# Optimization experiments

Measured on AMD Instinct MI355X. Metric: run time of the kernel, lower is better.

## Reference

```python
import jax, jax.numpy as jnp
import numpy as np

BETA = 0.9
THR = 1.0
NUM_STEPS = 10
SLOPE = 25.0


def spike(x):
    # forward-only heaviside (surrogate grad handled in fwdbwd module)
    return (x > 0).astype(x.dtype)


def setup_inputs() -> dict:
    key = jax.random.key(0)
    ks = jax.random.split(key, 7)
    B = 131072
    x = jax.random.normal(ks[0], (B, 250), dtype=jnp.float32)
    W1 = jax.random.normal(ks[1], (256, 250), dtype=jnp.float32) * 0.06
    b1 = jax.random.normal(ks[2], (256,), dtype=jnp.float32) * 0.06
    W2 = jax.random.normal(ks[3], (128, 256), dtype=jnp.float32) * 0.06
    b2 = jax.random.normal(ks[4], (128,), dtype=jnp.float32) * 0.06
    W3 = jax.random.normal(ks[5], (5, 128), dtype=jnp.float32) * 0.09
    b3 = jax.random.normal(ks[6], (5,), dtype=jnp.float32) * 0.09
    return {"x": x, "W1": W1, "b1": b1, "W2": W2, "b2": b2, "W3": W3, "b3": b3}


def reference(x, W1, b1, W2, b2, W3, b3):
    B = x.shape[0]
    # cur1 is identical every step (input x is static) -> hoist out of loop
    cur1 = x @ W1.T + b1  # [B, 256]

    def step(carry, _):
        m1, m2, m3, acc = carry
        # snntorch Leaky (reset_mechanism='subtract'):
        # reset from incoming mem (detached), then decay+input-reset, then fire
        r1 = (m1 > THR).astype(x.dtype)
        m1 = BETA * m1 + cur1 - r1 * THR
        s1 = spike(m1 - THR)

        cur2 = s1 @ W2.T + b2  # [B, 128]
        r2 = (m2 > THR).astype(x.dtype)
        m2 = BETA * m2 + cur2 - r2 * THR
        s2 = spike(m2 - THR)

        cur3 = s2 @ W3.T + b3  # [B, 5]
        r3 = (m3 > THR).astype(x.dtype)
        m3 = BETA * m3 + cur3 - r3 * THR
        s3 = spike(m3 - THR)

        return (m1, m2, m3, acc + s3), None

    init = (
        jnp.zeros((B, 256), x.dtype),
        jnp.zeros((B, 128), x.dtype),
        jnp.zeros((B, 5), x.dtype),
        jnp.zeros((B, 5), x.dtype),
    )
    (_, _, _, acc), _ = jax.lax.scan(step, init, None, length=NUM_STEPS)
    return acc  # sum of output spikes over timesteps, [B, 5]
```

## Files before the change

### kernel.cpp

```cpp
#include <hip/hip_runtime.h>

#define NSTEP 10

typedef __attribute__((ext_vector_type(8))) short bf16x8;
typedef __attribute__((ext_vector_type(4))) float f32x4;

extern "C" __global__ void __launch_bounds__(256) snn_prep(
    const float* __restrict__ W1, float* __restrict__ W1T)
{
    int i0 = blockIdx.x * 256 + threadIdx.x;
    int stride = gridDim.x * 256;
    for (int idx = i0; idx < 250 * 256; idx += stride) {
        int k = idx >> 8;
        int n = idx & 255;
        W1T[idx] = W1[n * 250 + k];
    }
}

__device__ __forceinline__ unsigned int bf16_rne_hi(float f) {
    unsigned int u = __float_as_uint(f);
    return (u + 0x7FFFu + ((u >> 16) & 1u)) & 0xFFFF0000u;
}

extern "C" __global__ void __launch_bounds__(256) snn_prep2(
    const float* __restrict__ W2, unsigned short* __restrict__ W2F)
{
    int idx = blockIdx.x * 256 + threadIdx.x;
    if (idx >= 8 * 3 * 8 * 64) return;
    int lane  = idx & 63;
    int slab  = (idx >> 6) & 7;
    int split = (idx >> 9) % 3;
    int w     = idx / (3 * 8 * 64);
    int j  = w * 16 + (lane & 15);
    int k0 = slab * 32 + (lane >> 4) * 8;
    unsigned short res[8];
    #pragma unroll
    for (int e = 0; e < 8; ++e) {
        float wval = W2[j * 256 + k0 + e];
        unsigned int u1 = bf16_rne_hi(wval);
        float r1 = __fsub_rn(wval, __uint_as_float(u1));
        unsigned int u2 = bf16_rne_hi(r1);
        float r2 = __fsub_rn(r1, __uint_as_float(u2));
        unsigned int u3 = bf16_rne_hi(r2);
        unsigned int sel = (split == 0) ? u1 : (split == 1) ? u2 : u3;
        res[e] = (unsigned short)(sel >> 16);
    }
    *(uint4*)&W2F[(((w * 3 + split) * 8 + slab) << 9) + lane * 8] =
        *(uint4*)res;
}

extern "C" __global__ void __launch_bounds__(256) snn_cur1(
    const float* __restrict__ x,
    const float* __restrict__ b1,
    const float* __restrict__ W1T,
    float* __restrict__ curG)
{
    __shared__ __align__(16) float xT[250 * 36];
    __shared__ __align__(16) float W1c[25 * 256];
    const int t   = threadIdx.x;
    const int nt  = t & 15;
    const int st  = t >> 4;
    const int s0a = st * 2;
    const int nt4 = nt * 4;
    const int sBase = blockIdx.x * 32;

    for (int i = t; i < 32 * 250; i += 256) {
        int sl = i / 250;
        int kl = i - sl * 250;
        xT[kl * 36 + sl] = x[(sBase + sl) * 250 + kl];
    }

    float rs[25];
    #pragma unroll
    for (int j = 0; j < 25; ++j) rs[j] = W1T[j * 256 + t];

    float cur1[4][4][2];
    #pragma unroll
    for (int j = 0; j < 4; ++j)
        #pragma unroll
        for (int e = 0; e < 4; ++e) { cur1[j][e][0] = 0.0f; cur1[j][e][1] = 0.0f; }

    __syncthreads();

    for (int c = 0; c < 10; ++c) {
        #pragma unroll
        for (int j = 0; j < 25; ++j) W1c[j * 256 + t] = rs[j];
        if (c < 9) {
            const float* src = W1T + (c + 1) * 6400;
            #pragma unroll
            for (int j = 0; j < 25; ++j) rs[j] = src[j * 256 + t];
        }
        __syncthreads();

        #pragma unroll 5
        for (int kl = 0; kl < 25; ++kl) {
            const int k = c * 25 + kl;
            const float2 xp = *(const float2*)&xT[k * 36 + s0a];
            float w[16];
            *(float4*)&w[0]  = *(const float4*)&W1c[kl * 256 +   0 + nt4];
            *(float4*)&w[4]  = *(const float4*)&W1c[kl * 256 +  64 + nt4];
            *(float4*)&w[8]  = *(const float4*)&W1c[kl * 256 + 128 + nt4];
            *(float4*)&w[12] = *(const float4*)&W1c[kl * 256 + 192 + nt4];
            #pragma unroll
            for (int j = 0; j < 4; ++j)
                #pragma unroll
                for (int e = 0; e < 4; ++e) {
                    cur1[j][e][0] = fmaf(w[j * 4 + e], xp.x, cur1[j][e][0]);
                    cur1[j][e][1] = fmaf(w[j * 4 + e], xp.y, cur1[j][e][1]);
                }
        }
        if (c < 9) __syncthreads();
    }

    {
        float bb[16];
        #pragma unroll
        for (int j = 0; j < 4; ++j)
            *(float4*)&bb[j * 4] = *(const float4*)&b1[j * 64 + nt4];
        #pragma unroll
        for (int j = 0; j < 4; ++j)
            #pragma unroll
            for (int e = 0; e < 4; ++e) {
                cur1[j][e][0] = __fadd_rn(cur1[j][e][0], bb[j * 4 + e]);
                cur1[j][e][1] = __fadd_rn(cur1[j][e][1], bb[j * 4 + e]);
            }
    }
    #pragma unroll
    for (int s = 0; s < 2; ++s)
        #pragma unroll
        for (int j = 0; j < 4; ++j) {
            *(float4*)&curG[(size_t)(sBase + s0a + s) * 256 + j * 64 + nt4] =
                make_float4(cur1[j][0][s], cur1[j][1][s],
                            cur1[j][2][s], cur1[j][3][s]);
        }
}

extern "C" __global__ void __launch_bounds__(512, 2) snn_main_split(
    const float* __restrict__ curG,
    const float* __restrict__ b2g,
    const float* __restrict__ W3,
    const float* __restrict__ b3,
    const unsigned short* __restrict__ W2F,
    float* __restrict__ out)
{
    __shared__ __align__(16) char ldsraw[51736];
    char* s1bf = ldsraw;
    unsigned char* s2Lb = (unsigned char*)(ldsraw + 32768);
    float* W3L = (float*)(ldsraw + 41984);
    float* pL  = (float*)(ldsraw + 46080);
    float* bL  = (float*)(ldsraw + 51200);

    const int t    = threadIdx.x;
    const int nt   = t & 15;
    const int st   = t >> 4;
    const int s0a  = st * 2;
    const int n0   = nt * 16;
    const int lane = t & 63;
    const int wv   = t >> 6;
    const int l15  = lane & 15;
    const int lq   = lane >> 4;
    const int sBase = blockIdx.x * 64;

    float cur1[16][2];
    #pragma unroll
    for (int s = 0; s < 2; ++s) {
        const float4* cp =
            (const float4*)&curG[(size_t)(sBase + s0a + s) * 256 + n0];
        float4 a = cp[0], b = cp[1], c = cp[2], d = cp[3];
        cur1[0][s] = a.x;  cur1[1][s] = a.y;  cur1[2][s] = a.z;  cur1[3][s] = a.w;
        cur1[4][s] = b.x;  cur1[5][s] = b.y;  cur1[6][s] = b.z;  cur1[7][s] = b.w;
        cur1[8][s] = c.x;  cur1[9][s] = c.y;  cur1[10][s] = c.z; cur1[11][s] = c.w;
        cur1[12][s] = d.x; cur1[13][s] = d.y; cur1[14][s] = d.z; cur1[15][s] = d.w;
    }

    for (int idx = t; idx < 640; idx += 512) {
        int o = idx >> 7;
        int j = idx & 127;
        W3L[j * 8 + o] = W3[idx];
    }
    if (t < 128) bL[t] = b2g[t];
    if (t < 5)   bL[128 + t] = b3[t];
    __syncthreads();

    float m1[16][2];
    #pragma unroll
    for (int i = 0; i < 16; ++i) { m1[i][0] = 0.0f; m1[i][1] = 0.0f; }
    float m2[4][4];
    #pragma unroll
    for (int mt = 0; mt < 4; ++mt)
        #pragma unroll
        for (int rg = 0; rg < 4; ++rg) m2[mt][rg] = 0.0f;
    float m3 = 0.0f, acc3 = 0.0f;

    const unsigned short* fb = W2F + (wv * 24) * 512 + lane * 8;
    const int keyB   = (lane & 7) << 4;
    const int chunkq = lq << 4;
    const int jC     = wv * 16 + l15;
    const int keyC2  = ((jC >> 2) & 7) << 3;

    #pragma unroll 1
    for (int stp = 0; stp < NSTEP; ++stp) {
        {
            unsigned int dwa[2][8];
            #pragma unroll
            for (int i = 0; i < 16; ++i) {
                #pragma unroll
                for (int s = 0; s < 2; ++s) {
                    float m = m1[i][s];
                    float r = (m > 1.0f) ? 1.0f : 0.0f;
                    m = __fsub_rn(__fadd_rn(__fmul_rn(0.9f, m), cur1[i][s]), r);
                    m1[i][s] = m;
                    unsigned int bits = (m > 1.0f) ? 0x3F80u : 0u;
                    if (i & 1) dwa[s][i >> 1] |= bits << 16;
                    else       dwa[s][i >> 1]  = bits;
                }
            }
            #pragma unroll
            for (int s = 0; s < 2; ++s) {
                const int row = s0a + s;
                const int key = row & 7;
                char* rp = s1bf + row * 512;
                uint4 lo = make_uint4(dwa[s][0], dwa[s][1], dwa[s][2], dwa[s][3]);
                uint4 hi = make_uint4(dwa[s][4], dwa[s][5], dwa[s][6], dwa[s][7]);
                *(uint4*)(rp + (((2 * nt + 0) ^ key) << 4)) = lo;
                *(uint4*)(rp + (((2 * nt + 1) ^ key) << 4)) = hi;
            }
        }
        __syncthreads();

        f32x4 acc[4];
        {
            const f32x4 z = {0.0f, 0.0f, 0.0f, 0.0f};
            acc[0] = z; acc[1] = z; acc[2] = z; acc[3] = z;
        }
        #pragma unroll
        for (int slab = 0; slab < 8; ++slab) {
            const bf16x8 B2 = *(const bf16x8*)(fb + (16 + slab) * 512);
            const bf16x8 B1 = *(const bf16x8*)(fb + (8  + slab) * 512);
            const bf16x8 B0 = *(const bf16x8*)(fb + (0  + slab) * 512);
            const int coff = (slab * 64 + chunkq) ^ keyB;
            const bf16x8 A0 = *(const bf16x8*)(s1bf + (l15     ) * 512 + coff);
            const bf16x8 A1 = *(const bf16x8*)(s1bf + (l15 + 16) * 512 + coff);
            const bf16x8 A2 = *(const bf16x8*)(s1bf + (l15 + 32) * 512 + coff);
            const bf16x8 A3 = *(const bf16x8*)(s1bf + (l15 + 48) * 512 + coff);
            acc[0] = __builtin_amdgcn_mfma_f32_16x16x32_bf16(A0, B2, acc[0], 0, 0, 0);
            acc[1] = __builtin_amdgcn_mfma_f32_16x16x32_bf16(A1, B2, acc[1], 0, 0, 0);
            acc[2] = __builtin_amdgcn_mfma_f32_16x16x32_bf16(A2, B2, acc[2], 0, 0, 0);
            acc[3] = __builtin_amdgcn_mfma_f32_16x16x32_bf16(A3, B2, acc[3], 0, 0, 0);
            acc[0] = __builtin_amdgcn_mfma_f32_16x16x32_bf16(A0, B1, acc[0], 0, 0, 0);
            acc[1] = __builtin_amdgcn_mfma_f32_16x16x32_bf16(A1, B1, acc[1], 0, 0, 0);
            acc[2] = __builtin_amdgcn_mfma_f32_16x16x32_bf16(A2, B1, acc[2], 0, 0, 0);
            acc[3] = __builtin_amdgcn_mfma_f32_16x16x32_bf16(A3, B1, acc[3], 0, 0, 0);
            acc[0] = __builtin_amdgcn_mfma_f32_16x16x32_bf16(A0, B0, acc[0], 0, 0, 0);
            acc[1] = __builtin_amdgcn_mfma_f32_16x16x32_bf16(A1, B0, acc[1], 0, 0, 0);
            acc[2] = __builtin_amdgcn_mfma_f32_16x16x32_bf16(A2, B0, acc[2], 0, 0, 0);
            acc[3] = __builtin_amdgcn_mfma_f32_16x16x32_bf16(A3, B0, acc[3], 0, 0, 0);
        }

        {
            const float bj = bL[jC];
            #pragma unroll
            for (int mt = 0; mt < 4; ++mt) {
                unsigned int pk = 0;
                #pragma unroll
                for (int rg = 0; rg < 4; ++rg) {
                    float c2 = __fadd_rn(acc[mt][rg], bj);
                    float m = m2[mt][rg];
                    float r = (m > 1.0f) ? 1.0f : 0.0f;
                    m = __fsub_rn(__fadd_rn(__fmul_rn(0.9f, m), c2), r);
                    m2[mt][rg] = m;
                    if (m > 1.0f) pk |= 1u << (8 * rg);
                }
                const int smp0 = mt * 16 + lq * 4;
                *(unsigned int*)&s2Lb[jC * 72 + (smp0 ^ keyC2)] = pk;
            }
        }
        __syncthreads();

        if (t < 256) {
            const int sl = t & 63;
            const int jr = t >> 6;
            float part[5] = {0.0f, 0.0f, 0.0f, 0.0f, 0.0f};
            #pragma unroll 8
            for (int jj = 0; jj < 32; ++jj) {
                const int j = jr * 32 + jj;
                const float s2v =
                    (float)s2Lb[j * 72 + (sl ^ (((j >> 2) & 7) << 3))];
                const float4 w3a = *(const float4*)&W3L[j * 8];
                const float  w3e = W3L[j * 8 + 4];
                part[0] = fmaf(w3a.x, s2v, part[0]);
                part[1] = fmaf(w3a.y, s2v, part[1]);
                part[2] = fmaf(w3a.z, s2v, part[2]);
                part[3] = fmaf(w3a.w, s2v, part[3]);
                part[4] = fmaf(w3e,   s2v, part[4]);
            }
            #pragma unroll
            for (int o = 0; o < 5; ++o)
                pL[(o * 4 + jr) * 64 + sl] = part[o];
        }
        __syncthreads();

        if (t < 320) {
            const int o  = t >> 6;
            const int sl = t & 63;
            float c3 = pL[(o * 4 + 0) * 64 + sl];
            c3 += pL[(o * 4 + 1) * 64 + sl];
            c3 += pL[(o * 4 + 2) * 64 + sl];
            c3 += pL[(o * 4 + 3) * 64 + sl];
            c3 = __fadd_rn(c3, bL[128 + o]);
            float m = m3;
            float r = (m > 1.0f) ? 1.0f : 0.0f;
            m = __fsub_rn(__fadd_rn(__fmul_rn(0.9f, m), c3), r);
            m3 = m;
            if (m > 1.0f) acc3 += 1.0f;
        }
    }

    if (t < 320) {
        out[(sBase + (t & 63)) * 5 + (t >> 6)] = acc3;
    }
}

extern "C" __global__ void __launch_bounds__(512, 2) snn_main_fused(
    const float* __restrict__ x,
    const float* __restrict__ b1,
    const float* __restrict__ b2g,
    const float* __restrict__ W3,
    const float* __restrict__ b3,
    const float* __restrict__ W1T,
    const unsigned short* __restrict__ W2F,
    float* __restrict__ out)
{
    __shared__ __align__(16) char ldsraw[68000];
    char* s1bf = ldsraw;
    unsigned char* s2Lb = (unsigned char*)(ldsraw + 32768);
    float* W3L = (float*)(ldsraw + 41984);
    float* pL  = (float*)(ldsraw + 46080);
    float* bL  = (float*)(ldsraw + 51200);
    float* xT  = (float*)(ldsraw);

    const int t    = threadIdx.x;
    const int nt   = t & 15;
    const int st   = t >> 4;
    const int s0a  = st * 2;
    const int n0   = nt * 16;
    const int lane = t & 63;
    const int wv   = t >> 6;
    const int l15  = lane & 15;
    const int lq   = lane >> 4;
    const int sBase = blockIdx.x * 64;

    for (int i = t; i < 64 * 250; i += 512) {
        int sl = i / 250;
        int kl = i - sl * 250;
        xT[kl * 68 + sl] = x[(sBase + sl) * 250 + kl];
    }
    __syncthreads();

    float cur1[16][2];
    #pragma unroll
    for (int i = 0; i < 16; ++i) { cur1[i][0] = 0.0f; cur1[i][1] = 0.0f; }

    #pragma unroll 5
    for (int k = 0; k < 250; ++k) {
        const float2 xp = *(const float2*)&xT[k * 68 + s0a];
        const float x0 = xp.x;
        const float x1 = xp.y;
        float w[16];
        *(float4*)&w[0]  = *(const float4*)&W1T[k * 256 + n0];
        *(float4*)&w[4]  = *(const float4*)&W1T[k * 256 + n0 + 4];
        *(float4*)&w[8]  = *(const float4*)&W1T[k * 256 + n0 + 8];
        *(float4*)&w[12] = *(const float4*)&W1T[k * 256 + n0 + 12];
        #pragma unroll
        for (int i = 0; i < 16; ++i) {
            cur1[i][0] = fmaf(w[i], x0, cur1[i][0]);
            cur1[i][1] = fmaf(w[i], x1, cur1[i][1]);
        }
    }
    {
        float bb[16];
        *(float4*)&bb[0]  = *(const float4*)&b1[n0];
        *(float4*)&bb[4]  = *(const float4*)&b1[n0 + 4];
        *(float4*)&bb[8]  = *(const float4*)&b1[n0 + 8];
        *(float4*)&bb[12] = *(const float4*)&b1[n0 + 12];
        #pragma unroll
        for (int i = 0; i < 16; ++i) {
            cur1[i][0] = __fadd_rn(cur1[i][0], bb[i]);
            cur1[i][1] = __fadd_rn(cur1[i][1], bb[i]);
        }
    }
    __syncthreads();

    for (int idx = t; idx < 640; idx += 512) {
        int o = idx >> 7;
        int j = idx & 127;
        W3L[j * 8 + o] = W3[idx];
    }
    if (t < 128) bL[t] = b2g[t];
    if (t < 5)   bL[128 + t] = b3[t];
    __syncthreads();

    float m1[16][2];
    #pragma unroll
    for (int i = 0; i < 16; ++i) { m1[i][0] = 0.0f; m1[i][1] = 0.0f; }
    float m2[4][4];
    #pragma unroll
    for (int mt = 0; mt < 4; ++mt)
        #pragma unroll
        for (int rg = 0; rg < 4; ++rg) m2[mt][rg] = 0.0f;
    float m3 = 0.0f, acc3 = 0.0f;

    const unsigned short* fb = W2F + (wv * 24) * 512 + lane * 8;
    const int keyB   = (lane & 7) << 4;
    const int chunkq = lq << 4;
    const int jC     = wv * 16 + l15;
    const int keyC2  = ((jC >> 2) & 7) << 3;

    #pragma unroll 1
    for (int stp = 0; stp < NSTEP; ++stp) {
        {
            unsigned int dwa[2][8];
            #pragma unroll
            for (int i = 0; i < 16; ++i) {
                #pragma unroll
                for (int s = 0; s < 2; ++s) {
                    float m = m1[i][s];
                    float r = (m > 1.0f) ? 1.0f : 0.0f;
                    m = __fsub_rn(__fadd_rn(__fmul_rn(0.9f, m), cur1[i][s]), r);
                    m1[i][s] = m;
                    unsigned int bits = (m > 1.0f) ? 0x3F80u : 0u;
                    if (i & 1) dwa[s][i >> 1] |= bits << 16;
                    else       dwa[s][i >> 1]  = bits;
                }
            }
            #pragma unroll
            for (int s = 0; s < 2; ++s) {
                const int row = s0a + s;
                const int key = row & 7;
                char* rp = s1bf + row * 512;
                uint4 lo = make_uint4(dwa[s][0], dwa[s][1], dwa[s][2], dwa[s][3]);
                uint4 hi = make_uint4(dwa[s][4], dwa[s][5], dwa[s][6], dwa[s][7]);
                *(uint4*)(rp + (((2 * nt + 0) ^ key) << 4)) = lo;
                *(uint4*)(rp + (((2 * nt + 1) ^ key) << 4)) = hi;
            }
        }
        __syncthreads();

        f32x4 acc[4];
        {
            const f32x4 z = {0.0f, 0.0f, 0.0f, 0.0f};
            acc[0] = z; acc[1] = z; acc[2] = z; acc[3] = z;
        }
        #pragma unroll
        for (int slab = 0; slab < 8; ++slab) {
            const bf16x8 B2 = *(const bf16x8*)(fb + (16 + slab) * 512);
            const bf16x8 B1 = *(const bf16x8*)(fb + (8  + slab) * 512);
            const bf16x8 B0 = *(const bf16x8*)(fb + (0  + slab) * 512);
            const int coff = (slab * 64 + chunkq) ^ keyB;
            const bf16x8 A0 = *(const bf16x8*)(s1bf + (l15     ) * 512 + coff);
            const bf16x8 A1 = *(const bf16x8*)(s1bf + (l15 + 16) * 512 + coff);
            const bf16x8 A2 = *(const bf16x8*)(s1bf + (l15 + 32) * 512 + coff);
            const bf16x8 A3 = *(const bf16x8*)(s1bf + (l15 + 48) * 512 + coff);
            acc[0] = __builtin_amdgcn_mfma_f32_16x16x32_bf16(A0, B2, acc[0], 0, 0, 0);
            acc[1] = __builtin_amdgcn_mfma_f32_16x16x32_bf16(A1, B2, acc[1], 0, 0, 0);
            acc[2] = __builtin_amdgcn_mfma_f32_16x16x32_bf16(A2, B2, acc[2], 0, 0, 0);
            acc[3] = __builtin_amdgcn_mfma_f32_16x16x32_bf16(A3, B2, acc[3], 0, 0, 0);
            acc[0] = __builtin_amdgcn_mfma_f32_16x16x32_bf16(A0, B1, acc[0], 0, 0, 0);
            acc[1] = __builtin_amdgcn_mfma_f32_16x16x32_bf16(A1, B1, acc[1], 0, 0, 0);
            acc[2] = __builtin_amdgcn_mfma_f32_16x16x32_bf16(A2, B1, acc[2], 0, 0, 0);
            acc[3] = __builtin_amdgcn_mfma_f32_16x16x32_bf16(A3, B1, acc[3], 0, 0, 0);
            acc[0] = __builtin_amdgcn_mfma_f32_16x16x32_bf16(A0, B0, acc[0], 0, 0, 0);
            acc[1] = __builtin_amdgcn_mfma_f32_16x16x32_bf16(A1, B0, acc[1], 0, 0, 0);
            acc[2] = __builtin_amdgcn_mfma_f32_16x16x32_bf16(A2, B0, acc[2], 0, 0, 0);
            acc[3] = __builtin_amdgcn_mfma_f32_16x16x32_bf16(A3, B0, acc[3], 0, 0, 0);
        }

        {
            const float bj = bL[jC];
            #pragma unroll
            for (int mt = 0; mt < 4; ++mt) {
                unsigned int pk = 0;
                #pragma unroll
                for (int rg = 0; rg < 4; ++rg) {
                    float c2 = __fadd_rn(acc[mt][rg], bj);
                    float m = m2[mt][rg];
                    float r = (m > 1.0f) ? 1.0f : 0.0f;
                    m = __fsub_rn(__fadd_rn(__fmul_rn(0.9f, m), c2), r);
                    m2[mt][rg] = m;
                    if (m > 1.0f) pk |= 1u << (8 * rg);
                }
                const int smp0 = mt * 16 + lq * 4;
                *(unsigned int*)&s2Lb[jC * 72 + (smp0 ^ keyC2)] = pk;
            }
        }
        __syncthreads();

        if (t < 256) {
            const int sl = t & 63;
            const int jr = t >> 6;
            float part[5] = {0.0f, 0.0f, 0.0f, 0.0f, 0.0f};
            #pragma unroll 8
            for (int jj = 0; jj < 32; ++jj) {
                const int j = jr * 32 + jj;
                const float s2v =
                    (float)s2Lb[j * 72 + (sl ^ (((j >> 2) & 7) << 3))];
                const float4 w3a = *(const float4*)&W3L[j * 8];
                const float  w3e = W3L[j * 8 + 4];
                part[0] = fmaf(w3a.x, s2v, part[0]);
                part[1] = fmaf(w3a.y, s2v, part[1]);
                part[2] = fmaf(w3a.z, s2v, part[2]);
                part[3] = fmaf(w3a.w, s2v, part[3]);
                part[4] = fmaf(w3e,   s2v, part[4]);
            }
            #pragma unroll
            for (int o = 0; o < 5; ++o)
                pL[(o * 4 + jr) * 64 + sl] = part[o];
        }
        __syncthreads();

        if (t < 320) {
            const int o  = t >> 6;
            const int sl = t & 63;
            float c3 = pL[(o * 4 + 0) * 64 + sl];
            c3 += pL[(o * 4 + 1) * 64 + sl];
            c3 += pL[(o * 4 + 2) * 64 + sl];
            c3 += pL[(o * 4 + 3) * 64 + sl];
            c3 = __fadd_rn(c3, bL[128 + o]);
            float m = m3;
            float r = (m > 1.0f) ? 1.0f : 0.0f;
            m = __fsub_rn(__fadd_rn(__fmul_rn(0.9f, m), c3), r);
            m3 = m;
            if (m > 1.0f) acc3 += 1.0f;
        }
    }

    if (t < 320) {
        out[(sBase + (t & 63)) * 5 + (t >> 6)] = acc3;
    }
}

extern "C" void kernel_launch(void* const* d_in, const int* in_sizes, int n_in,
                              void* d_out, int out_size, void* d_ws, size_t ws_size,
                              hipStream_t stream) {
    const float* x  = (const float*)d_in[0];
    const float* W1 = (const float*)d_in[1];
    const float* b1 = (const float*)d_in[2];
    const float* W2 = (const float*)d_in[3];
    const float* b2 = (const float*)d_in[4];
    const float* W3 = (const float*)d_in[5];
    const float* b3 = (const float*)d_in[6];
    float* out = (float*)d_out;

    float* W1T = (float*)d_ws;
    unsigned short* W2F = (unsigned short*)((char*)d_ws + 262144);

    const int B = in_sizes[0] / 250;
    const size_t curBytes = (size_t)B * 256 * sizeof(float);
    const size_t curOff   = 262144 + 196608;

    snn_prep <<<64, 256, 0, stream>>>(W1, W1T);
    snn_prep2<<<48, 256, 0, stream>>>(W2, W2F);

    if (ws_size >= curOff + curBytes) {
        float* curG = (float*)((char*)d_ws + curOff);
        snn_cur1<<<B / 32, 256, 0, stream>>>(x, b1, W1T, curG);
        snn_main_split<<<B / 64, 512, 0, stream>>>(curG, b2, W3, b3, W2F, out);
    } else {
        snn_main_fused<<<B / 64, 512, 0, stream>>>(x, b1, b2, W3, b3, W1T, W2F,
                                                   out);
    }
}
```

Baseline: 644.9 us.

## Stage cur1 in LDS, double-buffer x chunks, and prefetch W2 fragments

In the cur1 kernel, the full transposed x tile in shared memory is replaced by a double-buffered 25-column chunk loaded through registers alongside the W1 chunk. This shrinks LDS use and overlaps global loads with compute. In the split main kernel, cur1 values move from registers to a swizzled LDS region (117 KB per block) and are reloaded every step, aimed at freeing VGPRs. The W2 fragment loads in the MFMA loop are software-pipelined two slabs ahead. The larger LDS footprint may prevent two blocks per CU, despite the launch bounds.

```diff
diff --git a/kernel.cpp b/kernel.cpp
--- a/kernel.cpp
+++ b/kernel.cpp
@@ -55,8 +55,8 @@
     const float* __restrict__ W1T,
     float* __restrict__ curG)
 {
-    __shared__ __align__(16) float xT[250 * 36];
     __shared__ __align__(16) float W1c[25 * 256];
+    __shared__ __align__(16) float xc[2][25 * 36];
     const int t   = threadIdx.x;
     const int nt  = t & 15;
     const int st  = t >> 4;
@@ -64,15 +64,15 @@
     const int nt4 = nt * 4;
     const int sBase = blockIdx.x * 32;
 
-    for (int i = t; i < 32 * 250; i += 256) {
-        int sl = i / 250;
-        int kl = i - sl * 250;
-        xT[kl * 36 + sl] = x[(sBase + sl) * 250 + kl];
-    }
-
+    for (int i = t; i < 800; i += 256) {
+        int sl = i / 25;
+        int e  = i - sl * 25;
+        xc[0][e * 36 + sl] = x[(size_t)(sBase + sl) * 250 + e];
+    }
     float rs[25];
     #pragma unroll
     for (int j = 0; j < 25; ++j) rs[j] = W1T[j * 256 + t];
+    float xs[4] = {0.0f, 0.0f, 0.0f, 0.0f};
 
     float cur1[4][4][2];
     #pragma unroll
@@ -85,17 +85,37 @@
     for (int c = 0; c < 10; ++c) {
         #pragma unroll
         for (int j = 0; j < 25; ++j) W1c[j * 256 + t] = rs[j];
+        if (c > 0) {
+            #pragma unroll
+            for (int r = 0; r < 4; ++r) {
+                int i = t + 256 * r;
+                if (i < 800) {
+                    int sl = i / 25;
+                    int e  = i - sl * 25;
+                    xc[c & 1][e * 36 + sl] = xs[r];
+                }
+            }
+        }
         if (c < 9) {
-            const float* src = W1T + (c + 1) * 6400;
-            #pragma unroll
-            for (int j = 0; j < 25; ++j) rs[j] = src[j * 256 + t];
+            const float* srcW = W1T + (c + 1) * 6400;
+            #pragma unroll
+            for (int j = 0; j < 25; ++j) rs[j] = srcW[j * 256 + t];
+            #pragma unroll
+            for (int r = 0; r < 4; ++r) {
+                int i = t + 256 * r;
+                if (i < 800) {
+                    int sl = i / 25;
+                    int e  = i - sl * 25;
+                    xs[r] = x[(size_t)(sBase + sl) * 250 + (c + 1) * 25 + e];
+                }
+            }
         }
         __syncthreads();
 
+        const float* xrow = &xc[c & 1][0];
         #pragma unroll 5
         for (int kl = 0; kl < 25; ++kl) {
-            const int k = c * 25 + kl;
-            const float2 xp = *(const float2*)&xT[k * 36 + s0a];
+            const float2 xp = *(const float2*)&xrow[kl * 36 + s0a];
             float w[16];
             *(float4*)&w[0]  = *(const float4*)&W1c[kl * 256 +   0 + nt4];
             *(float4*)&w[4]  = *(const float4*)&W1c[kl * 256 +  64 + nt4];
@@ -143,12 +163,13 @@
     const unsigned short* __restrict__ W2F,
     float* __restrict__ out)
 {
-    __shared__ __align__(16) char ldsraw[51736];
-    char* s1bf = ldsraw;
-    unsigned char* s2Lb = (unsigned char*)(ldsraw + 32768);
-    float* W3L = (float*)(ldsraw + 41984);
-    float* pL  = (float*)(ldsraw + 46080);
-    float* bL  = (float*)(ldsraw + 51200);
+    __shared__ __align__(16) char ldsraw[117280];
+    float* cur1L = (float*)(ldsraw);
+    char* s1bf = ldsraw + 65536;
+    unsigned char* s2Lb = (unsigned char*)(ldsraw + 98304);
+    float* W3L = (float*)(ldsraw + 107520);
+    float* pL  = (float*)(ldsraw + 111616);
+    float* bL  = (float*)(ldsraw + 116736);
 
     const int t    = threadIdx.x;
     const int nt   = t & 15;
@@ -160,18 +181,259 @@
     const int l15  = lane & 15;
     const int lq   = lane >> 4;
     const int sBase = blockIdx.x * 64;
-
-    float cur1[16][2];
+    const int tk   = t & 7;
+    float* myc = cur1L + t * 32;
+
     #pragma unroll
     for (int s = 0; s < 2; ++s) {
         const float4* cp =
             (const float4*)&curG[(size_t)(sBase + s0a + s) * 256 + n0];
-        float4 a = cp[0], b = cp[1], c = cp[2], d = cp[3];
-        cur1[0][s] = a.x;  cur1[1][s] = a.y;  cur1[2][s] = a.z;  cur1[3][s] = a.w;
-        cur1[4][s] = b.x;  cur1[5][s] = b.y;  cur1[6][s] = b.z;  cur1[7][s] = b.w;
-        cur1[8][s] = c.x;  cur1[9][s] = c.y;  cur1[10][s] = c.z; cur1[11][s] = c.w;
-        cur1[12][s] = d.x; cur1[13][s] = d.y; cur1[14][s] = d.z; cur1[15][s] = d.w;
-    }
+        #pragma unroll
+        for (int q = 0; q < 4; ++q) {
+            float4 v = cp[q];
+            *(float4*)&myc[((s * 4 + q) ^ tk) * 4] = v;
+        }
+    }
+
+    for (int idx = t; idx < 640; idx += 512) {
+        int o = idx >> 7;
+        int j = idx & 127;
+        W3L[j * 8 + o] = W3[idx];
+    }
+    if (t < 128) bL[t] = b2g[t];
+    if (t < 5)   bL[128 + t] = b3[t];
+    __syncthreads();
+
+    float m1[16][2];
+    #pragma unroll
+    for (int i = 0; i < 16; ++i) { m1[i][0] = 0.0f; m1[i][1] = 0.0f; }
+    float m2[4][4];
+    #pragma unroll
+    for (int mt = 0; mt < 4; ++mt)
+        #pragma unroll
+        for (int rg = 0; rg < 4; ++rg) m2[mt][rg] = 0.0f;
+    float m3 = 0.0f, acc3 = 0.0f;
+
+    const unsigned short* fb = W2F + (wv * 24) * 512 + lane * 8;
+    const int keyB   = (lane & 7) << 4;
+    const int chunkq = lq << 4;
+    const int jC     = wv * 16 + l15;
+    const int keyC2  = ((jC >> 2) & 7) << 3;
+
+    #pragma unroll 1
+    for (int stp = 0; stp < NSTEP; ++stp) {
+        {
+            float c1v[16][2];
+            #pragma unroll
+            for (int s = 0; s < 2; ++s)
+                #pragma unroll
+                for (int q = 0; q < 4; ++q) {
+                    float4 v = *(const float4*)&myc[((s * 4 + q) ^ tk) * 4];
+                    c1v[q * 4 + 0][s] = v.x;
+                    c1v[q * 4 + 1][s] = v.y;
+                    c1v[q * 4 + 2][s] = v.z;
+                    c1v[q * 4 + 3][s] = v.w;
+                }
+            unsigned int dwa[2][8];
+            #pragma unroll
+            for (int i = 0; i < 16; ++i) {
+                #pragma unroll
+                for (int s = 0; s < 2; ++s) {
+                    float m = m1[i][s];
+                    float r = (m > 1.0f) ? 1.0f : 0.0f;
+                    m = __fsub_rn(__fadd_rn(__fmul_rn(0.9f, m), c1v[i][s]), r);
+                    m1[i][s] = m;
+                    unsigned int bits = (m > 1.0f) ? 0x3F80u : 0u;
+                    if (i & 1) dwa[s][i >> 1] |= bits << 16;
+                    else       dwa[s][i >> 1]  = bits;
+                }
+            }
+            #pragma unroll
+            for (int s = 0; s < 2; ++s) {
+                const int row = s0a + s;
+                const int key = row & 7;
+                char* rp = s1bf + row * 512;
+                uint4 lo = make_uint4(dwa[s][0], dwa[s][1], dwa[s][2], dwa[s][3]);
+                uint4 hi = make_uint4(dwa[s][4], dwa[s][5], dwa[s][6], dwa[s][7]);
+                *(uint4*)(rp + (((2 * nt + 0) ^ key) << 4)) = lo;
+                *(uint4*)(rp + (((2 * nt + 1) ^ key) << 4)) = hi;
+            }
+        }
+        __syncthreads();
+
+        f32x4 acc[4];
+        {
+            const f32x4 z = {0.0f, 0.0f, 0.0f, 0.0f};
+            acc[0] = z; acc[1] = z; acc[2] = z; acc[3] = z;
+        }
+        bf16x8 B2c = *(const bf16x8*)(fb + (16 + 0) * 512);
+        bf16x8 B1c = *(const bf16x8*)(fb + (8  + 0) * 512);
+        bf16x8 B0c = *(const bf16x8*)(fb + (0  + 0) * 512);
+        bf16x8 B2n = *(const bf16x8*)(fb + (16 + 1) * 512);
+        bf16x8 B1n = *(const bf16x8*)(fb + (8  + 1) * 512);
+        bf16x8 B0n = *(const bf16x8*)(fb + (0  + 1) * 512);
+        #pragma unroll
+        for (int slab = 0; slab < 8; ++slab) {
+            bf16x8 B2f, B1f, B0f;
+            if (slab < 6) {
+                B2f = *(const bf16x8*)(fb + (16 + slab + 2) * 512);
+                B1f = *(const bf16x8*)(fb + (8  + slab + 2) * 512);
+                B0f = *(const bf16x8*)(fb + (0  + slab + 2) * 512);
+            }
+            const int coff = (slab * 64 + chunkq) ^ keyB;
+            const bf16x8 A0 = *(const bf16x8*)(s1bf + (l15     ) * 512 + coff);
+            const bf16x8 A1 = *(const bf16x8*)(s1bf + (l15 + 16) * 512 + coff);
+            const bf16x8 A2 = *(const bf16x8*)(s1bf + (l15 + 32) * 512 + coff);
+            const bf16x8 A3 = *(const bf16x8*)(s1bf + (l15 + 48) * 512 + coff);
+            acc[0] = __builtin_amdgcn_mfma_f32_16x16x32_bf16(A0, B2c, acc[0], 0, 0, 0);
+            acc[1] = __builtin_amdgcn_mfma_f32_16x16x32_bf16(A1, B2c, acc[1], 0, 0, 0);
+            acc[2] = __builtin_amdgcn_mfma_f32_16x16x32_bf16(A2, B2c, acc[2], 0, 0, 0);
+            acc[3] = __builtin_amdgcn_mfma_f32_16x16x32_bf16(A3, B2c, acc[3], 0, 0, 0);
+            acc[0] = __builtin_amdgcn_mfma_f32_16x16x32_bf16(A0, B1c, acc[0], 0, 0, 0);
+            acc[1] = __builtin_amdgcn_mfma_f32_16x16x32_bf16(A1, B1c, acc[1], 0, 0, 0);
+            acc[2] = __builtin_amdgcn_mfma_f32_16x16x32_bf16(A2, B1c, acc[2], 0, 0, 0);
+            acc[3] = __builtin_amdgcn_mfma_f32_16x16x32_bf16(A3, B1c, acc[3], 0, 0, 0);
+            acc[0] = __builtin_amdgcn_mfma_f32_16x16x32_bf16(A0, B0c, acc[0], 0, 0, 0);
+            acc[1] = __builtin_amdgcn_mfma_f32_16x16x32_bf16(A1, B0c, acc[1], 0, 0, 0);
+            acc[2] = __builtin_amdgcn_mfma_f32_16x16x32_bf16(A2, B0c, acc[2], 0, 0, 0);
+            acc[3] = __builtin_amdgcn_mfma_f32_16x16x32_bf16(A3, B0c, acc[3], 0, 0, 0);
+            if (slab < 7) { B2c = B2n; B1c = B1n; B0c = B0n; }
+            if (slab < 6) { B2n = B2f; B1n = B1f; B0n = B0f; }
+        }
+
+        {
+            const float bj = bL[jC];
+            #pragma unroll
+            for (int mt = 0; mt < 4; ++mt) {
+                unsigned int pk = 0;
+                #pragma unroll
+                for (int rg = 0; rg < 4; ++rg) {
+                    float c2 = __fadd_rn(acc[mt][rg], bj);
+                    float m = m2[mt][rg];
+                    float r = (m > 1.0f) ? 1.0f : 0.0f;
+                    m = __fsub_rn(__fadd_rn(__fmul_rn(0.9f, m), c2), r);
+                    m2[mt][rg] = m;
+                    if (m > 1.0f) pk |= 1u << (8 * rg);
+                }
+                const int smp0 = mt * 16 + lq * 4;
+                *(unsigned int*)&s2Lb[jC * 72 + (smp0 ^ keyC2)] = pk;
+            }
+        }
+        __syncthreads();
+
+        if (t < 256) {
+            const int sl = t & 63;
+            const int jr = t >> 6;
+            float part[5] = {0.0f, 0.0f, 0.0f, 0.0f, 0.0f};
+            #pragma unroll 8
+            for (int jj = 0; jj < 32; ++jj) {
+                const int j = jr * 32 + jj;
+                const float s2v =
+                    (float)s2Lb[j * 72 + (sl ^ (((j >> 2) & 7) << 3))];
+                const float4 w3a = *(const float4*)&W3L[j * 8];
+                const float  w3e = W3L[j * 8 + 4];
+                part[0] = fmaf(w3a.x, s2v, part[0]);
+                part[1] = fmaf(w3a.y, s2v, part[1]);
+                part[2] = fmaf(w3a.z, s2v, part[2]);
+                part[3] = fmaf(w3a.w, s2v, part[3]);
+                part[4] = fmaf(w3e,   s2v, part[4]);
+            }
+            #pragma unroll
+            for (int o = 0; o < 5; ++o)
+                pL[(o * 4 + jr) * 64 + sl] = part[o];
+        }
+        __syncthreads();
+
+        if (t < 320) {
+            const int o  = t >> 6;
+            const int sl = t & 63;
+            float c3 = pL[(o * 4 + 0) * 64 + sl];
+            c3 += pL[(o * 4 + 1) * 64 + sl];
+            c3 += pL[(o * 4 + 2) * 64 + sl];
+            c3 += pL[(o * 4 + 3) * 64 + sl];
+            c3 = __fadd_rn(c3, bL[128 + o]);
+            float m = m3;
+            float r = (m > 1.0f) ? 1.0f : 0.0f;
+            m = __fsub_rn(__fadd_rn(__fmul_rn(0.9f, m), c3), r);
+            m3 = m;
+            if (m > 1.0f) acc3 += 1.0f;
+        }
+    }
+
+    if (t < 320) {
+        out[(sBase + (t & 63)) * 5 + (t >> 6)] = acc3;
+    }
+}
+
+extern "C" __global__ void __launch_bounds__(512, 2) snn_main_fused(
+    const float* __restrict__ x,
+    const float* __restrict__ b1,
+    const float* __restrict__ b2g,
+    const float* __restrict__ W3,
+    const float* __restrict__ b3,
+    const float* __restrict__ W1T,
+    const unsigned short* __restrict__ W2F,
+    float* __restrict__ out)
+{
+    __shared__ __align__(16) char ldsraw[68000];
+    char* s1bf = ldsraw;
+    unsigned char* s2Lb = (unsigned char*)(ldsraw + 32768);
+    float* W3L = (float*)(ldsraw + 41984);
+    float* pL  = (float*)(ldsraw + 46080);
+    float* bL  = (float*)(ldsraw + 51200);
+    float* xT  = (float*)(ldsraw);
+
+    const int t    = threadIdx.x;
+    const int nt   = t & 15;
+    const int st   = t >> 4;
+    const int s0a  = st * 2;
+    const int n0   = nt * 16;
+    const int lane = t & 63;
+    const int wv   = t >> 6;
+    const int l15  = lane & 15;
+    const int lq   = lane >> 4;
+    const int sBase = blockIdx.x * 64;
+
+    for (int i = t; i < 64 * 250; i += 512) {
+        int sl = i / 250;
+        int kl = i - sl * 250;
+        xT[kl * 68 + sl] = x[(sBase + sl) * 250 + kl];
+    }
+    __syncthreads();
+
+    float cur1[16][2];
+    #pragma unroll
+    for (int i = 0; i < 16; ++i) { cur1[i][0] = 0.0f; cur1[i][1] = 0.0f; }
+
+    #pragma unroll 5
+    for (int k = 0; k < 250; ++k) {
+        const float2 xp = *(const float2*)&xT[k * 68 + s0a];
+        const float x0 = xp.x;
+        const float x1 = xp.y;
+        float w[16];
+        *(float4*)&w[0]  = *(const float4*)&W1T[k * 256 + n0];
+        *(float4*)&w[4]  = *(const float4*)&W1T[k * 256 + n0 + 4];
+        *(float4*)&w[8]  = *(const float4*)&W1T[k * 256 + n0 + 8];
+        *(float4*)&w[12] = *(const float4*)&W1T[k * 256 + n0 + 12];
+        #pragma unroll
+        for (int i = 0; i < 16; ++i) {
+            cur1[i][0] = fmaf(w[i], x0, cur1[i][0]);
+            cur1[i][1] = fmaf(w[i], x1, cur1[i][1]);
+        }
+    }
+    {
+        float bb[16];
+        *(float4*)&bb[0]  = *(const float4*)&b1[n0];
+        *(float4*)&bb[4]  = *(const float4*)&b1[n0 + 4];
+        *(float4*)&bb[8]  = *(const float4*)&b1[n0 + 8];
+        *(float4*)&bb[12] = *(const float4*)&b1[n0 + 12];
+        #pragma unroll
+        for (int i = 0; i < 16; ++i) {
+            cur1[i][0] = __fadd_rn(cur1[i][0], bb[i]);
+            cur1[i][1] = __fadd_rn(cur1[i][1], bb[i]);
+        }
+    }
+    __syncthreads();
 
     for (int idx = t; idx < 640; idx += 512) {
         int o = idx >> 7;
@@ -321,224 +583,6 @@
     }
 }
 
-extern "C" __global__ void __launch_bounds__(512, 2) snn_main_fused(
-    const float* __restrict__ x,
-    const float* __restrict__ b1,
-    const float* __restrict__ b2g,
-    const float* __restrict__ W3,
-    const float* __restrict__ b3,
-    const float* __restrict__ W1T,
-    const unsigned short* __restrict__ W2F,
-    float* __restrict__ out)
-{
-    __shared__ __align__(16) char ldsraw[68000];
-    char* s1bf = ldsraw;
-    unsigned char* s2Lb = (unsigned char*)(ldsraw + 32768);
-    float* W3L = (float*)(ldsraw + 41984);
-    float* pL  = (float*)(ldsraw + 46080);
-    float* bL  = (float*)(ldsraw + 51200);
-    float* xT  = (float*)(ldsraw);
-
-    const int t    = threadIdx.x;
-    const int nt   = t & 15;
-    const int st   = t >> 4;
-    const int s0a  = st * 2;
-    const int n0   = nt * 16;
-    const int lane = t & 63;
-    const int wv   = t >> 6;
-    const int l15  = lane & 15;
-    const int lq   = lane >> 4;
-    const int sBase = blockIdx.x * 64;
-
-    for (int i = t; i < 64 * 250; i += 512) {
-        int sl = i / 250;
-        int kl = i - sl * 250;
-        xT[kl * 68 + sl] = x[(sBase + sl) * 250 + kl];
-    }
-    __syncthreads();
-
-    float cur1[16][2];
-    #pragma unroll
-    for (int i = 0; i < 16; ++i) { cur1[i][0] = 0.0f; cur1[i][1] = 0.0f; }
-
-    #pragma unroll 5
-    for (int k = 0; k < 250; ++k) {
-        const float2 xp = *(const float2*)&xT[k * 68 + s0a];
-        const float x0 = xp.x;
-        const float x1 = xp.y;
-        float w[16];
-        *(float4*)&w[0]  = *(const float4*)&W1T[k * 256 + n0];
-        *(float4*)&w[4]  = *(const float4*)&W1T[k * 256 + n0 + 4];
-        *(float4*)&w[8]  = *(const float4*)&W1T[k * 256 + n0 + 8];
-        *(float4*)&w[12] = *(const float4*)&W1T[k * 256 + n0 + 12];
-        #pragma unroll
-        for (int i = 0; i < 16; ++i) {
-            cur1[i][0] = fmaf(w[i], x0, cur1[i][0]);
-            cur1[i][1] = fmaf(w[i], x1, cur1[i][1]);
-        }
-    }
-    {
-        float bb[16];
-        *(float4*)&bb[0]  = *(const float4*)&b1[n0];
-        *(float4*)&bb[4]  = *(const float4*)&b1[n0 + 4];
-        *(float4*)&bb[8]  = *(const float4*)&b1[n0 + 8];
-        *(float4*)&bb[12] = *(const float4*)&b1[n0 + 12];
-        #pragma unroll
-        for (int i = 0; i < 16; ++i) {
-            cur1[i][0] = __fadd_rn(cur1[i][0], bb[i]);
-            cur1[i][1] = __fadd_rn(cur1[i][1], bb[i]);
-        }
-    }
-    __syncthreads();
-
-    for (int idx = t; idx < 640; idx += 512) {
-        int o = idx >> 7;
-        int j = idx & 127;
-        W3L[j * 8 + o] = W3[idx];
-    }
-    if (t < 128) bL[t] = b2g[t];
-    if (t < 5)   bL[128 + t] = b3[t];
-    __syncthreads();
-
-    float m1[16][2];
-    #pragma unroll
-    for (int i = 0; i < 16; ++i) { m1[i][0] = 0.0f; m1[i][1] = 0.0f; }
-    float m2[4][4];
-    #pragma unroll
-    for (int mt = 0; mt < 4; ++mt)
-        #pragma unroll
-        for (int rg = 0; rg < 4; ++rg) m2[mt][rg] = 0.0f;
-    float m3 = 0.0f, acc3 = 0.0f;
-
-    const unsigned short* fb = W2F + (wv * 24) * 512 + lane * 8;
-    const int keyB   = (lane & 7) << 4;
-    const int chunkq = lq << 4;
-    const int jC     = wv * 16 + l15;
-    const int keyC2  = ((jC >> 2) & 7) << 3;
-
-    #pragma unroll 1
-    for (int stp = 0; stp < NSTEP; ++stp) {
-        {
-            unsigned int dwa[2][8];
-            #pragma unroll
-            for (int i = 0; i < 16; ++i) {
-                #pragma unroll
-                for (int s = 0; s < 2; ++s) {
-                    float m = m1[i][s];
-                    float r = (m > 1.0f) ? 1.0f : 0.0f;
-                    m = __fsub_rn(__fadd_rn(__fmul_rn(0.9f, m), cur1[i][s]), r);
-                    m1[i][s] = m;
-                    unsigned int bits = (m > 1.0f) ? 0x3F80u : 0u;
-                    if (i & 1) dwa[s][i >> 1] |= bits << 16;
-                    else       dwa[s][i >> 1]  = bits;
-                }
-            }
-            #pragma unroll
-            for (int s = 0; s < 2; ++s) {
-                const int row = s0a + s;
-                const int key = row & 7;
-                char* rp = s1bf + row * 512;
-                uint4 lo = make_uint4(dwa[s][0], dwa[s][1], dwa[s][2], dwa[s][3]);
-                uint4 hi = make_uint4(dwa[s][4], dwa[s][5], dwa[s][6], dwa[s][7]);
-                *(uint4*)(rp + (((2 * nt + 0) ^ key) << 4)) = lo;
-                *(uint4*)(rp + (((2 * nt + 1) ^ key) << 4)) = hi;
-            }
-        }
-        __syncthreads();
-
-        f32x4 acc[4];
-        {
-            const f32x4 z = {0.0f, 0.0f, 0.0f, 0.0f};
-            acc[0] = z; acc[1] = z; acc[2] = z; acc[3] = z;
-        }
-        #pragma unroll
-        for (int slab = 0; slab < 8; ++slab) {
-            const bf16x8 B2 = *(const bf16x8*)(fb + (16 + slab) * 512);
-            const bf16x8 B1 = *(const bf16x8*)(fb + (8  + slab) * 512);
-            const bf16x8 B0 = *(const bf16x8*)(fb + (0  + slab) * 512);
-            const int coff = (slab * 64 + chunkq) ^ keyB;
-            const bf16x8 A0 = *(const bf16x8*)(s1bf + (l15     ) * 512 + coff);
-            const bf16x8 A1 = *(const bf16x8*)(s1bf + (l15 + 16) * 512 + coff);
-            const bf16x8 A2 = *(const bf16x8*)(s1bf + (l15 + 32) * 512 + coff);
-            const bf16x8 A3 = *(const bf16x8*)(s1bf + (l15 + 48) * 512 + coff);
-            acc[0] = __builtin_amdgcn_mfma_f32_16x16x32_bf16(A0, B2, acc[0], 0, 0, 0);
-            acc[1] = __builtin_amdgcn_mfma_f32_16x16x32_bf16(A1, B2, acc[1], 0, 0, 0);
-            acc[2] = __builtin_amdgcn_mfma_f32_16x16x32_bf16(A2, B2, acc[2], 0, 0, 0);
-            acc[3] = __builtin_amdgcn_mfma_f32_16x16x32_bf16(A3, B2, acc[3], 0, 0, 0);
-            acc[0] = __builtin_amdgcn_mfma_f32_16x16x32_bf16(A0, B1, acc[0], 0, 0, 0);
-            acc[1] = __builtin_amdgcn_mfma_f32_16x16x32_bf16(A1, B1, acc[1], 0, 0, 0);
-            acc[2] = __builtin_amdgcn_mfma_f32_16x16x32_bf16(A2, B1, acc[2], 0, 0, 0);
-            acc[3] = __builtin_amdgcn_mfma_f32_16x16x32_bf16(A3, B1, acc[3], 0, 0, 0);
-            acc[0] = __builtin_amdgcn_mfma_f32_16x16x32_bf16(A0, B0, acc[0], 0, 0, 0);
-            acc[1] = __builtin_amdgcn_mfma_f32_16x16x32_bf16(A1, B0, acc[1], 0, 0, 0);
-            acc[2] = __builtin_amdgcn_mfma_f32_16x16x32_bf16(A2, B0, acc[2], 0, 0, 0);
-            acc[3] = __builtin_amdgcn_mfma_f32_16x16x32_bf16(A3, B0, acc[3], 0, 0, 0);
-        }
-
-        {
-            const float bj = bL[jC];
-            #pragma unroll
-            for (int mt = 0; mt < 4; ++mt) {
-                unsigned int pk = 0;
-                #pragma unroll
-                for (int rg = 0; rg < 4; ++rg) {
-                    float c2 = __fadd_rn(acc[mt][rg], bj);
-                    float m = m2[mt][rg];
-                    float r = (m > 1.0f) ? 1.0f : 0.0f;
-                    m = __fsub_rn(__fadd_rn(__fmul_rn(0.9f, m), c2), r);
-                    m2[mt][rg] = m;
-                    if (m > 1.0f) pk |= 1u << (8 * rg);
-                }
-                const int smp0 = mt * 16 + lq * 4;
-                *(unsigned int*)&s2Lb[jC * 72 + (smp0 ^ keyC2)] = pk;
-            }
-        }
-        __syncthreads();
-
-        if (t < 256) {
-            const int sl = t & 63;
-            const int jr = t >> 6;
-            float part[5] = {0.0f, 0.0f, 0.0f, 0.0f, 0.0f};
-            #pragma unroll 8
-            for (int jj = 0; jj < 32; ++jj) {
-                const int j = jr * 32 + jj;
-                const float s2v =
-                    (float)s2Lb[j * 72 + (sl ^ (((j >> 2) & 7) << 3))];
-                const float4 w3a = *(const float4*)&W3L[j * 8];
-                const float  w3e = W3L[j * 8 + 4];
-                part[0] = fmaf(w3a.x, s2v, part[0]);
-                part[1] = fmaf(w3a.y, s2v, part[1]);
-                part[2] = fmaf(w3a.z, s2v, part[2]);
-                part[3] = fmaf(w3a.w, s2v, part[3]);
-                part[4] = fmaf(w3e,   s2v, part[4]);
-            }
-            #pragma unroll
-            for (int o = 0; o < 5; ++o)
-                pL[(o * 4 + jr) * 64 + sl] = part[o];
-        }
-        __syncthreads();
-
-        if (t < 320) {
-            const int o  = t >> 6;
-            const int sl = t & 63;
-            float c3 = pL[(o * 4 + 0) * 64 + sl];
-            c3 += pL[(o * 4 + 1) * 64 + sl];
-            c3 += pL[(o * 4 + 2) * 64 + sl];
-            c3 += pL[(o * 4 + 3) * 64 + sl];
-            c3 = __fadd_rn(c3, bL[128 + o]);
-            float m = m3;
-            float r = (m > 1.0f) ? 1.0f : 0.0f;
-            m = __fsub_rn(__fadd_rn(__fmul_rn(0.9f, m), c3), r);
-            m3 = m;
-            if (m > 1.0f) acc3 += 1.0f;
-        }
-    }
-
-    if (t < 320) {
-        out[(sBase + (t & 63)) * 5 + (t >> 6)] = acc3;
-    }
-}
-
 extern "C" void kernel_launch(void* const* d_in, const int* in_sizes, int n_in,
                               void* d_out, int out_size, void* d_ws, size_t ws_size,
                               hipStream_t stream) {
```

New measurement: 591.0 us, median of 3. 8.4% less time.
